# Kernel tuning notes

Measured on AMD Instinct MI355X. Metric: run time of the kernel, lower is better.

## Reference

```python
import jax, jax.numpy as jnp
import numpy as np

B, N, E = 64, 1024, 16384  # graphs, nodes per graph, edges per graph
N_ITER = 5
NORMALIZE = True
NUM_INIT_LABELS = 16


def _unique_inverse(h):
    """Equivalent of torch.unique(h, sorted=True, return_inverse=True)[1] for 1-D h."""
    order = jnp.argsort(h)
    sh = h[order]
    bnd = jnp.concatenate([jnp.zeros(1, jnp.int32), (sh[1:] != sh[:-1]).astype(jnp.int32)])
    ranks = jnp.cumsum(bnd)  # dense rank in sorted-unique order
    return jnp.zeros_like(ranks).at[order].set(ranks)


def _wl_iteration(mask, labels, hash_w):
    """One WL iteration for all graphs.
    mask: [B,N,N] bool dense adjacency (sparse-to-dense, as in the torch code)
    labels: [B,N] int32
    hash_w: [2] float32 (Linear(2,1,bias=False) weight)
    Returns new labels [B,N] int32.
    """
    w0, w1 = hash_w[0], hash_w[1]
    lab_f = labels.astype(jnp.float32)
    deg = mask.sum(-1).astype(jnp.float32)                      # [B,N] valid-neighbor count
    K = deg.max(axis=-1, keepdims=True)                         # per-graph max_neighbors
    # sum of neighbor labels (gather+reduce over the dense mask, memory-bound)
    seg = jnp.einsum('bij,bj->bi', mask.astype(jnp.float32), lab_f)  # [B,N]
    # torch builds [N,max_neighbors] rows: node label in col 0-feature, sorted
    # neighbor labels (padded with -1) in col 1-feature, hashes each pair with
    # w0*node + w1*neigh and sums over columns. Closed form (sort is sum-invariant):
    #   K*w0*node + w1*(sum_neighbors - (K - deg))
    hashed = K * w0 * lab_f + w1 * (seg + deg - K)              # [B,N]
    return jax.vmap(_unique_inverse)(hashed)


def setup_inputs() -> dict:
    key = jax.random.key(0)
    k1, k2, k3, k4 = jax.random.split(key, 4)
    edge_src = jax.random.randint(k1, (B, E), 0, N, dtype=jnp.int32)
    edge_dst = jax.random.randint(k2, (B, E), 0, N, dtype=jnp.int32)
    labels = jax.random.randint(k3, (B, N), 0, NUM_INIT_LABELS, dtype=jnp.int32)
    hash_w = jax.random.normal(k4, (2,), dtype=jnp.float32)
    return {"edge_src": edge_src, "edge_dst": edge_dst, "labels": labels, "hash_w": hash_w}


def reference(edge_src, edge_dst, labels, hash_w):
    # sparse-to-dense neighbor mask, as in the torch module
    b_idx = jnp.arange(B, dtype=jnp.int32)[:, None]
    mask = jnp.zeros((B, N, N), dtype=bool).at[b_idx, edge_src, edge_dst].set(True)

    all_labels = [labels]
    for _ in range(N_ITER):
        all_labels.append(_wl_iteration(mask, all_labels[-1], hash_w))

    # feature vectors: per graph, bincount of labels summed over all iterations.
    # Labels are always < N (unique-inverse ranks < N; initial labels < 16),
    # so N bins is a tight static upper bound for torch's max_label+1; the extra
    # zero columns do not change the Gram matrix.
    labels_all = jnp.stack(all_labels, axis=1).reshape(B, -1)   # [B, (n_iter+1)*N]
    feats = jax.vmap(lambda l: jnp.zeros((N,), jnp.float32).at[l].add(1.0))(labels_all)

    kernel = feats @ feats.T                                    # [B,B]
    if NORMALIZE:
        d = jnp.sqrt(jnp.diag(kernel))
        kernel = kernel / (d[None, :] * d[:, None])
    return kernel
```

## Files before the change

kernel.cpp:

```cpp
#include <hip/hip_runtime.h>

#define B 64
#define N 1024
#define E 16384
#define WPR 32
#define NITER 5
#define CSR_SLOTS (E + N)
#define MAXP 20
#define SENT_PAIR 0x04000400u

#define FEATS_OFF 0
#define DIAG_OFF  ((size_t)B * N * 4)

__global__ void __launch_bounds__(1024) wl_mega_k(const int* __restrict__ src,
                                                  const int* __restrict__ dstp,
                                                  const int* __restrict__ lab0,
                                                  const float* __restrict__ hw,
                                                  unsigned int* __restrict__ feats,
                                                  float* __restrict__ diag) {
    __shared__ union {
        unsigned int chunk[N * WPR];
        struct {
            unsigned short nbr[CSR_SLOTS];
            struct {
                int hist[N];
                int scan[N];
                float grp[N];
                int flag[N];
            } pb;
        } s;
    } u;
    __shared__ int s_lab[N + 2];
    __shared__ unsigned int s_feats[N];
    __shared__ int s_wsum[16];
    __shared__ int s_kp[16];
    __shared__ float s_mn[16], s_mx[16];
    __shared__ int s_anytie;
    int b = blockIdx.x, t = threadIdx.x;
    int lane = t & 63, w = t >> 6;

    const int* sg = src + (size_t)b * E;
    const int* dg_ = dstp + (size_t)b * E;
    int es[16], ed[16];
#pragma unroll
    for (int k = 0; k < 16; ++k) {
        es[k] = sg[t + k * 1024];
        ed[k] = dg_[t + k * 1024];
    }
    int l0 = lab0[(size_t)b * N + t];
    float w0 = hw[0], w1 = hw[1];
#pragma unroll
    for (int k = 0; k < 8; ++k)
        ((uint4*)u.chunk)[t + k * 1024] = make_uint4(0, 0, 0, 0);
    s_lab[t] = l0;
    s_feats[t] = 0;
    if (t == 0) { s_lab[N] = 0; s_anytie = 0; }
    __syncthreads();
#pragma unroll
    for (int v = 0; v < 16; ++v) {
        unsigned long long m = __ballot(l0 == v);
        if (lane == v) {
            int c = __popcll(m);
            if (c) atomicAdd(&s_feats[v], (unsigned)c);
        }
    }

#pragma unroll
    for (int k = 0; k < 16; ++k) {
        int wlog = ed[k] >> 5;
        int g = wlog >> 2;
        int p = (g + es[k]) & 7;
        atomicOr(&u.chunk[es[k] * WPR + p * 4 + (wlog & 3)], 1u << (ed[k] & 31));
    }
    __syncthreads();
    uint4 r[8];
    {
        const uint4* row4 = (const uint4*)(u.chunk + t * WPR);
#pragma unroll
        for (int g = 0; g < 8; ++g)
            r[g] = row4[(g + t) & 7];
    }
    __syncthreads();

    int dg = 0;
#pragma unroll
    for (int k = 0; k < 8; ++k)
        dg += __popc(r[k].x) + __popc(r[k].y) + __popc(r[k].z) + __popc(r[k].w);
    int alloc = (dg + 1) & ~1;

    int f = alloc;
#pragma unroll
    for (int d2 = 1; d2 < 64; d2 <<= 1) {
        int v = __shfl_up(f, d2);
        if (lane >= d2) f += v;
    }
    int km = dg;
#pragma unroll
    for (int o = 32; o > 0; o >>= 1) km = max(km, __shfl_down(km, o));
    if (lane == 63) s_wsum[w] = f;
    if (lane == 0)  s_kp[w] = km;
    __syncthreads();
    float Kf;
    int start;
    {
        int vv = ((lane & 15) < w) ? s_wsum[lane & 15] : 0;
#pragma unroll
        for (int m2 = 1; m2 < 16; m2 <<= 1) vv += __shfl_xor(vv, m2);
        start = (f - alloc) + vv;
        int kk = s_kp[lane & 15];
#pragma unroll
        for (int m2 = 8; m2 >= 1; m2 >>= 1) kk = max(kk, __shfl_xor(kk, m2));
        Kf = (float)kk;
    }
    u.s.pb.hist[t] = 0;
    u.s.pb.flag[t] = 0;

    {
        int idx = start;
#pragma unroll
        for (int k = 0; k < 8; ++k) {
            unsigned int wv[4] = { r[k].x, r[k].y, r[k].z, r[k].w };
#pragma unroll
            for (int c2 = 0; c2 < 4; ++c2) {
                unsigned int word = wv[c2];
                int bb = (k * 4 + c2) << 5;
                while (word) {
                    int j = __ffs(word) - 1;
                    word &= word - 1;
                    u.s.nbr[idx++] = (unsigned short)(bb + j);
                }
            }
        }
        if (dg & 1) u.s.nbr[idx] = (unsigned short)N;
    }
    __syncthreads();

    int vdeg = dg;
    int vpstart = start >> 1;
    int vpairs = alloc >> 1;
    int lab_reg = l0;
    const unsigned int* nbr32 = (const unsigned int*)u.s.nbr;
    unsigned int pw[MAXP];
#pragma unroll
    for (int k = 0; k < MAXP; ++k)
        pw[k] = (k < vpairs) ? nbr32[vpstart + k] : SENT_PAIR;

    int nfast = 0;
    for (int it = 0; it < NITER; ++it) {
        int ssum = 0;
#pragma unroll
        for (int k = 0; k < MAXP; ++k) {
            unsigned int pr = pw[k];
            ssum += s_lab[pr & 0xFFFFu] + s_lab[pr >> 16];
        }
        for (int k = MAXP; k < vpairs; ++k) {
            unsigned int pr = nbr32[vpstart + k];
            ssum += s_lab[pr & 0xFFFFu] + s_lab[pr >> 16];
        }
        float t1 = __fmul_rn(__fmul_rn(Kf, w0), (float)lab_reg);
        float t2 = __fmul_rn(w1, __fsub_rn(__fadd_rn((float)ssum, (float)vdeg), Kf));
        float h  = __fadd_rn(t1, t2);

        float mn = h, mx = h;
#pragma unroll
        for (int o = 32; o > 0; o >>= 1) {
            mn = fminf(mn, __shfl_down(mn, o));
            mx = fmaxf(mx, __shfl_down(mx, o));
        }
        if (lane == 0) { s_mn[w] = mn; s_mx[w] = mx; }
        __syncthreads();
        float fmn, span;
        {
            float a = s_mn[lane & 15];
            float cmx = s_mx[lane & 15];
#pragma unroll
            for (int m2 = 8; m2 >= 1; m2 >>= 1) {
                a = fminf(a, __shfl_xor(a, m2));
                cmx = fmaxf(cmx, __shfl_xor(cmx, m2));
            }
            fmn = a;
            span = cmx - a;
        }
        float scale = (span > 0.f) ? (1023.0f / span) : 0.f;
        int bucket = min((int)((h - fmn) * scale), 1023);
        int off_in = atomicAdd(&u.s.pb.hist[bucket], 1);
        __syncthreads();

        f = u.s.pb.hist[t];
#pragma unroll
        for (int d2 = 1; d2 < 64; d2 <<= 1) {
            int v = __shfl_up(f, d2);
            if (lane >= d2) f += v;
        }
        if (lane == 63) s_wsum[w] = f;
        __syncthreads();
        {
            int vv = ((lane & 15) < w) ? s_wsum[lane & 15] : 0;
#pragma unroll
            for (int m2 = 1; m2 < 16; m2 <<= 1) vv += __shfl_xor(vv, m2);
            u.s.pb.scan[t] = f + vv;
        }
        __syncthreads();

        int bs = u.s.pb.scan[bucket] - u.s.pb.hist[bucket];
        int be = u.s.pb.scan[bucket];
        u.s.pb.grp[bs + off_in] = h;
        __syncthreads();

        int cr = bs;
        int eq = 0;
        for (int k = bs; k < be; ++k) {
            float g = u.s.pb.grp[k];
            cr += (g < h);
            eq += (g == h);
        }
        if (eq > 1) s_anytie = it + 1;
        u.s.pb.hist[t] = 0;
        s_lab[t] = cr;
        __syncthreads();
        if (s_anytie == it + 1) {
            u.s.pb.flag[cr] = 1;
            __syncthreads();
            int f2 = u.s.pb.flag[t];
#pragma unroll
            for (int d2 = 1; d2 < 64; d2 <<= 1) {
                int v = __shfl_up(f2, d2);
                if (lane >= d2) f2 += v;
            }
            if (lane == 63) s_wsum[w] = f2;
            __syncthreads();
            {
                int vv = ((lane & 15) < w) ? s_wsum[lane & 15] : 0;
#pragma unroll
                for (int m2 = 1; m2 < 16; m2 <<= 1) vv += __shfl_xor(vv, m2);
                u.s.pb.scan[t] = f2 + vv;
            }
            u.s.pb.flag[t] = 0;
            __syncthreads();
            int rank = u.s.pb.scan[cr] - 1;
            s_lab[t] = rank;
            lab_reg = rank;
            atomicAdd(&s_feats[rank], 1u);
            __syncthreads();
        } else {
            lab_reg = cr;
            ++nfast;
        }
    }

    unsigned int fv = s_feats[t] + (unsigned)nfast;
    feats[(size_t)b * N + t] = fv;
    int sq = (int)(fv * fv);
#pragma unroll
    for (int o = 32; o > 0; o >>= 1) sq += __shfl_down(sq, o);
    if (lane == 0) s_wsum[w] = sq;
    __syncthreads();
    if (t == 0) {
        int tot = 0;
#pragma unroll
        for (int k = 0; k < 16; ++k) tot += s_wsum[k];
        diag[b] = (float)tot;
    }
}

__global__ void __launch_bounds__(1024) gram_k(const unsigned int* __restrict__ feats,
                                               const float* __restrict__ diag,
                                               float* __restrict__ out) {
    __shared__ unsigned int s_fi[N];
    int i = blockIdx.x, t = threadIdx.x;
    int lane = t & 63, w = t >> 6;
    if (t < 256)
        ((uint4*)s_fi)[t] = ((const uint4*)(feats + (size_t)i * N))[t];
    __syncthreads();
    float di = diag[i];
#pragma unroll
    for (int jj = 0; jj < 4; ++jj) {
        int j = w * 4 + jj;
        const uint4* fj = (const uint4*)(feats + (size_t)j * N);
        const uint4* fi = (const uint4*)s_fi;
        int s = 0;
#pragma unroll
        for (int k = 0; k < 4; ++k) {
            uint4 vb = fj[lane + k * 64];
            uint4 va = fi[lane + k * 64];
            s += (int)(va.x * vb.x) + (int)(va.y * vb.y)
               + (int)(va.z * vb.z) + (int)(va.w * vb.w);
        }
#pragma unroll
        for (int off = 32; off > 0; off >>= 1) s += __shfl_down(s, off);
        if (lane == 0) out[i * B + j] = (float)s / sqrtf(di * diag[j]);
    }
}

extern "C" void kernel_launch(void* const* d_in, const int* in_sizes, int n_in,
                              void* d_out, int out_size, void* d_ws, size_t ws_size,
                              hipStream_t stream) {
    const int*   esrc = (const int*)d_in[0];
    const int*   edst = (const int*)d_in[1];
    const int*   lab0 = (const int*)d_in[2];
    const float* hw   = (const float*)d_in[3];

    char* ws = (char*)d_ws;
    unsigned int* feats = (unsigned int*)(ws + FEATS_OFF);
    float*        diag  = (float*)(ws + DIAG_OFF);

    wl_mega_k<<<B, 1024, 0, stream>>>(esrc, edst, lab0, hw, feats, diag);
    gram_k<<<B, 1024, 0, stream>>>(feats, diag, (float*)d_out);
}
```

Before: 99.25 us.

## Split CSR construction into a separate 4-blocks-per-graph pre-kernel

Adjacency bitmap and CSR building move out of the per-graph mega kernel into a new kernel that runs 256 blocks, each handling 256 source rows of one graph. It writes fixed-stride (32-word) CSR rows, degrees, per-quarter max degree and an overflow flag to workspace. The main kernel then loads its neighbor pairs from global memory and skips the bitmap and scan work, falling back to the old in-block path only when a row exceeds 62 neighbors. The aim is to spread the setup phase over more CUs than the 64 blocks used before, at the cost of an extra launch and a global round trip for the CSR data.

```diff
diff --git a/kernel.cpp b/kernel.cpp
--- a/kernel.cpp
+++ b/kernel.cpp
@@ -8,14 +8,110 @@
 #define CSR_SLOTS (E + N)
 #define MAXP 20
 #define SENT_PAIR 0x04000400u
+#define CSR_STRIDE 32
 
 #define FEATS_OFF 0
 #define DIAG_OFF  ((size_t)B * N * 4)
+#define CSR_OFF   ((size_t)1 << 20)
+#define DEG_OFF   (CSR_OFF + (size_t)B * N * CSR_STRIDE * 4)
+#define KPART_OFF (DEG_OFF + (size_t)B * N * 4)
+#define OVFP_OFF  (KPART_OFF + 4096)
+
+__global__ void __launch_bounds__(1024) csr_k(const int* __restrict__ src,
+                                              const int* __restrict__ dstp,
+                                              unsigned int* __restrict__ csr,
+                                              unsigned int* __restrict__ degarr,
+                                              unsigned int* __restrict__ kpart,
+                                              unsigned int* __restrict__ ovfp) {
+    __shared__ unsigned int bm[256 * WPR];
+    __shared__ int s_kp[16];
+    __shared__ int s_ovf;
+    int blk = blockIdx.x, t = threadIdx.x;
+    int lane = t & 63, w = t >> 6;
+    int b = blk >> 2, q = blk & 3, base = q << 8;
+
+#pragma unroll
+    for (int k = 0; k < 2; ++k)
+        ((uint4*)bm)[t + k * 1024] = make_uint4(0, 0, 0, 0);
+    if (t == 0) s_ovf = 0;
+    __syncthreads();
+
+    const int* sg = src + (size_t)b * E;
+    const int* dgp = dstp + (size_t)b * E;
+#pragma unroll
+    for (int k = 0; k < 16; ++k) {
+        int es = sg[t + k * 1024];
+        int ed = dgp[t + k * 1024];
+        int rr = es - base;
+        if ((unsigned)rr < 256u) {
+            int wlog = ed >> 5;
+            int g = wlog >> 2;
+            int p = (g + rr) & 7;
+            atomicOr(&bm[rr * WPR + p * 4 + (wlog & 3)], 1u << (ed & 31));
+        }
+    }
+    __syncthreads();
+
+    int r = t >> 2, sub = t & 3;
+    const uint4* row4 = (const uint4*)(bm + r * WPR);
+    uint4 ra = row4[(sub * 2 + r) & 7];
+    uint4 rb = row4[(sub * 2 + 1 + r) & 7];
+    int pdeg = __popc(ra.x) + __popc(ra.y) + __popc(ra.z) + __popc(ra.w)
+             + __popc(rb.x) + __popc(rb.y) + __popc(rb.z) + __popc(rb.w);
+    int d01 = pdeg + __shfl_xor(pdeg, 1);
+    int deg = d01 + __shfl_xor(d01, 2);
+    int pre = 0;
+    {
+        int v1 = __shfl_up(pdeg, 1); if ((lane & 3) >= 1) pre += v1;
+        int v2 = __shfl_up(pdeg, 2); if ((lane & 3) >= 2) pre += v2;
+        int v3 = __shfl_up(pdeg, 3); if ((lane & 3) >= 3) pre += v3;
+    }
+    int node = b * N + base + r;
+    if (sub == 0) degarr[node] = (unsigned)deg;
+    if (deg <= 62) {
+        unsigned short* row16 = (unsigned short*)(csr + (size_t)node * CSR_STRIDE);
+        int idx = pre;
+        unsigned int wv[8] = { ra.x, ra.y, ra.z, ra.w, rb.x, rb.y, rb.z, rb.w };
+#pragma unroll
+        for (int c = 0; c < 8; ++c) {
+            unsigned int word = wv[c];
+            int gg = sub * 2 + (c >> 2);
+            int bb = (gg * 4 + (c & 3)) << 5;
+            while (word) {
+                int j = __ffs(word) - 1;
+                word &= word - 1;
+                row16[idx++] = (unsigned short)(bb + j);
+            }
+        }
+        if (sub == 0) {
+            row16[deg] = (unsigned short)N;
+            row16[deg + 1] = (unsigned short)N;
+        }
+    } else {
+        s_ovf = 1;
+    }
+    int km = deg;
+#pragma unroll
+    for (int o = 32; o > 0; o >>= 1) km = max(km, __shfl_down(km, o));
+    if (lane == 0) s_kp[w] = km;
+    __syncthreads();
+    if (t == 0) {
+        int kk = 0;
+#pragma unroll
+        for (int k = 0; k < 16; ++k) kk = max(kk, s_kp[k]);
+        kpart[blk] = (unsigned)kk;
+        ovfp[blk] = (unsigned)s_ovf;
+    }
+}
 
 __global__ void __launch_bounds__(1024) wl_mega_k(const int* __restrict__ src,
                                                   const int* __restrict__ dstp,
                                                   const int* __restrict__ lab0,
                                                   const float* __restrict__ hw,
+                                                  const unsigned int* __restrict__ csr,
+                                                  const unsigned int* __restrict__ degarr,
+                                                  const unsigned int* __restrict__ kpart,
+                                                  const unsigned int* __restrict__ ovfp,
                                                   unsigned int* __restrict__ feats,
                                                   float* __restrict__ diag) {
     __shared__ union {
@@ -39,111 +135,137 @@
     int b = blockIdx.x, t = threadIdx.x;
     int lane = t & 63, w = t >> 6;
 
-    const int* sg = src + (size_t)b * E;
-    const int* dg_ = dstp + (size_t)b * E;
-    int es[16], ed[16];
-#pragma unroll
-    for (int k = 0; k < 16; ++k) {
-        es[k] = sg[t + k * 1024];
-        ed[k] = dg_[t + k * 1024];
-    }
     int l0 = lab0[(size_t)b * N + t];
     float w0 = hw[0], w1 = hw[1];
-#pragma unroll
-    for (int k = 0; k < 8; ++k)
-        ((uint4*)u.chunk)[t + k * 1024] = make_uint4(0, 0, 0, 0);
-    s_lab[t] = l0;
-    s_feats[t] = 0;
-    if (t == 0) { s_lab[N] = 0; s_anytie = 0; }
-    __syncthreads();
-#pragma unroll
-    for (int v = 0; v < 16; ++v) {
-        unsigned long long m = __ballot(l0 == v);
-        if (lane == v) {
-            int c = __popcll(m);
-            if (c) atomicAdd(&s_feats[v], (unsigned)c);
-        }
-    }
-
-#pragma unroll
-    for (int k = 0; k < 16; ++k) {
-        int wlog = ed[k] >> 5;
-        int g = wlog >> 2;
-        int p = (g + es[k]) & 7;
-        atomicOr(&u.chunk[es[k] * WPR + p * 4 + (wlog & 3)], 1u << (ed[k] & 31));
-    }
-    __syncthreads();
-    uint4 r[8];
-    {
-        const uint4* row4 = (const uint4*)(u.chunk + t * WPR);
-#pragma unroll
-        for (int g = 0; g < 8; ++g)
-            r[g] = row4[(g + t) & 7];
-    }
-    __syncthreads();
-
-    int dg = 0;
-#pragma unroll
-    for (int k = 0; k < 8; ++k)
-        dg += __popc(r[k].x) + __popc(r[k].y) + __popc(r[k].z) + __popc(r[k].w);
-    int alloc = (dg + 1) & ~1;
-
-    int f = alloc;
-#pragma unroll
-    for (int d2 = 1; d2 < 64; d2 <<= 1) {
-        int v = __shfl_up(f, d2);
-        if (lane >= d2) f += v;
-    }
-    int km = dg;
-#pragma unroll
-    for (int o = 32; o > 0; o >>= 1) km = max(km, __shfl_down(km, o));
-    if (lane == 63) s_wsum[w] = f;
-    if (lane == 0)  s_kp[w] = km;
-    __syncthreads();
+    uint4 ov = *((const uint4*)(ovfp + (b << 2)));
+    uint4 kq = *((const uint4*)(kpart + (b << 2)));
+    int ovfg = (int)(ov.x | ov.y | ov.z | ov.w);
+
+    int vdeg, vpairs;
     float Kf;
-    int start;
-    {
-        int vv = ((lane & 15) < w) ? s_wsum[lane & 15] : 0;
-#pragma unroll
-        for (int m2 = 1; m2 < 16; m2 <<= 1) vv += __shfl_xor(vv, m2);
-        start = (f - alloc) + vv;
-        int kk = s_kp[lane & 15];
-#pragma unroll
-        for (int m2 = 8; m2 >= 1; m2 >>= 1) kk = max(kk, __shfl_xor(kk, m2));
-        Kf = (float)kk;
-    }
-    u.s.pb.hist[t] = 0;
-    u.s.pb.flag[t] = 0;
-
-    {
-        int idx = start;
-#pragma unroll
-        for (int k = 0; k < 8; ++k) {
-            unsigned int wv[4] = { r[k].x, r[k].y, r[k].z, r[k].w };
-#pragma unroll
-            for (int c2 = 0; c2 < 4; ++c2) {
-                unsigned int word = wv[c2];
-                int bb = (k * 4 + c2) << 5;
-                while (word) {
-                    int j = __ffs(word) - 1;
-                    word &= word - 1;
-                    u.s.nbr[idx++] = (unsigned short)(bb + j);
+    int lab_reg = l0;
+    unsigned int pw[MAXP];
+    const unsigned int* p_fb;
+
+    if (!ovfg) {
+        vdeg = (int)degarr[(size_t)b * N + t];
+        vpairs = (vdeg + 1) >> 1;
+        Kf = (float)max(max(kq.x, kq.y), max(kq.z, kq.w));
+        const unsigned int* crow = csr + (size_t)(b * N + t) * CSR_STRIDE;
+        p_fb = crow;
+#pragma unroll
+        for (int k = 0; k < MAXP; ++k)
+            pw[k] = (k < vpairs) ? crow[k] : SENT_PAIR;
+        s_lab[t] = l0;
+        s_feats[t] = 0;
+        u.s.pb.hist[t] = 0;
+        u.s.pb.flag[t] = 0;
+        if (t == 0) { s_lab[N] = 0; s_anytie = 0; }
+        __syncthreads();
+#pragma unroll
+        for (int v = 0; v < 16; ++v) {
+            unsigned long long m = __ballot(l0 == v);
+            if (lane == v) {
+                int c = __popcll(m);
+                if (c) atomicAdd(&s_feats[v], (unsigned)c);
+            }
+        }
+    } else {
+        const int* sg = src + (size_t)b * E;
+        const int* dg_ = dstp + (size_t)b * E;
+        int es[16], ed[16];
+#pragma unroll
+        for (int k = 0; k < 16; ++k) {
+            es[k] = sg[t + k * 1024];
+            ed[k] = dg_[t + k * 1024];
+        }
+#pragma unroll
+        for (int k = 0; k < 8; ++k)
+            ((uint4*)u.chunk)[t + k * 1024] = make_uint4(0, 0, 0, 0);
+        s_lab[t] = l0;
+        s_feats[t] = 0;
+        if (t == 0) { s_lab[N] = 0; s_anytie = 0; }
+        __syncthreads();
+#pragma unroll
+        for (int v = 0; v < 16; ++v) {
+            unsigned long long m = __ballot(l0 == v);
+            if (lane == v) {
+                int c = __popcll(m);
+                if (c) atomicAdd(&s_feats[v], (unsigned)c);
+            }
+        }
+#pragma unroll
+        for (int k = 0; k < 16; ++k) {
+            int wlog = ed[k] >> 5;
+            int g = wlog >> 2;
+            int p = (g + es[k]) & 7;
+            atomicOr(&u.chunk[es[k] * WPR + p * 4 + (wlog & 3)], 1u << (ed[k] & 31));
+        }
+        __syncthreads();
+        uint4 r[8];
+        {
+            const uint4* row4 = (const uint4*)(u.chunk + t * WPR);
+#pragma unroll
+            for (int g = 0; g < 8; ++g)
+                r[g] = row4[(g + t) & 7];
+        }
+        __syncthreads();
+        int dg = 0;
+#pragma unroll
+        for (int k = 0; k < 8; ++k)
+            dg += __popc(r[k].x) + __popc(r[k].y) + __popc(r[k].z) + __popc(r[k].w);
+        int alloc = (dg + 1) & ~1;
+        int f = alloc;
+#pragma unroll
+        for (int d2 = 1; d2 < 64; d2 <<= 1) {
+            int v = __shfl_up(f, d2);
+            if (lane >= d2) f += v;
+        }
+        int km = dg;
+#pragma unroll
+        for (int o = 32; o > 0; o >>= 1) km = max(km, __shfl_down(km, o));
+        if (lane == 63) s_wsum[w] = f;
+        if (lane == 0)  s_kp[w] = km;
+        __syncthreads();
+        int start;
+        {
+            int vv = ((lane & 15) < w) ? s_wsum[lane & 15] : 0;
+#pragma unroll
+            for (int m2 = 1; m2 < 16; m2 <<= 1) vv += __shfl_xor(vv, m2);
+            start = (f - alloc) + vv;
+            int kk = s_kp[lane & 15];
+#pragma unroll
+            for (int m2 = 8; m2 >= 1; m2 >>= 1) kk = max(kk, __shfl_xor(kk, m2));
+            Kf = (float)kk;
+        }
+        u.s.pb.hist[t] = 0;
+        u.s.pb.flag[t] = 0;
+        {
+            int idx = start;
+#pragma unroll
+            for (int k = 0; k < 8; ++k) {
+                unsigned int wv[4] = { r[k].x, r[k].y, r[k].z, r[k].w };
+#pragma unroll
+                for (int c2 = 0; c2 < 4; ++c2) {
+                    unsigned int word = wv[c2];
+                    int bb = (k * 4 + c2) << 5;
+                    while (word) {
+                        int j = __ffs(word) - 1;
+                        word &= word - 1;
+                        u.s.nbr[idx++] = (unsigned short)(bb + j);
+                    }
                 }
             }
-        }
-        if (dg & 1) u.s.nbr[idx] = (unsigned short)N;
-    }
-    __syncthreads();
-
-    int vdeg = dg;
-    int vpstart = start >> 1;
-    int vpairs = alloc >> 1;
-    int lab_reg = l0;
-    const unsigned int* nbr32 = (const unsigned int*)u.s.nbr;
-    unsigned int pw[MAXP];
-#pragma unroll
-    for (int k = 0; k < MAXP; ++k)
-        pw[k] = (k < vpairs) ? nbr32[vpstart + k] : SENT_PAIR;
+            if (dg & 1) u.s.nbr[idx] = (unsigned short)N;
+        }
+        __syncthreads();
+        vdeg = dg;
+        vpairs = alloc >> 1;
+        p_fb = (const unsigned int*)u.s.nbr + (start >> 1);
+#pragma unroll
+        for (int k = 0; k < MAXP; ++k)
+            pw[k] = (k < vpairs) ? p_fb[k] : SENT_PAIR;
+    }
 
     int nfast = 0;
     for (int it = 0; it < NITER; ++it) {
@@ -154,7 +276,7 @@
             ssum += s_lab[pr & 0xFFFFu] + s_lab[pr >> 16];
         }
         for (int k = MAXP; k < vpairs; ++k) {
-            unsigned int pr = nbr32[vpstart + k];
+            unsigned int pr = p_fb[k];
             ssum += s_lab[pr & 0xFFFFu] + s_lab[pr >> 16];
         }
         float t1 = __fmul_rn(__fmul_rn(Kf, w0), (float)lab_reg);
@@ -186,7 +308,7 @@
         int off_in = atomicAdd(&u.s.pb.hist[bucket], 1);
         __syncthreads();
 
-        f = u.s.pb.hist[t];
+        int f = u.s.pb.hist[t];
 #pragma unroll
         for (int d2 = 1; d2 < 64; d2 <<= 1) {
             int v = __shfl_up(f, d2);
@@ -303,7 +425,13 @@
     char* ws = (char*)d_ws;
     unsigned int* feats = (unsigned int*)(ws + FEATS_OFF);
     float*        diag  = (float*)(ws + DIAG_OFF);
-
-    wl_mega_k<<<B, 1024, 0, stream>>>(esrc, edst, lab0, hw, feats, diag);
+    unsigned int* csr   = (unsigned int*)(ws + CSR_OFF);
+    unsigned int* degar = (unsigned int*)(ws + DEG_OFF);
+    unsigned int* kpart = (unsigned int*)(ws + KPART_OFF);
+    unsigned int* ovfp  = (unsigned int*)(ws + OVFP_OFF);
+
+    csr_k<<<B * 4, 1024, 0, stream>>>(esrc, edst, csr, degar, kpart, ovfp);
+    wl_mega_k<<<B, 1024, 0, stream>>>(esrc, edst, lab0, hw, csr, degar, kpart,
+                                      ovfp, feats, diag);
     gram_k<<<B, 1024, 0, stream>>>(feats, diag, (float*)d_out);
 }
```

New measurement: 111.2 us. 12.1% more time.
